# Kernel optimization log

Measured on AMD Instinct MI355X. Metric: run time of the kernel, lower is better.

The kernel has to match this reference:

```python
import jax, jax.numpy as jnp
import numpy as np

WS = 16       # window size
SHIFT = 8     # shift size
HEADS = 16
DIM = 512
HIDDEN = 2048
B, H, W = 8, 64, 64
EPS = 1e-5


def _rel_coords_table(ws):
    h = np.arange(-(ws - 1), ws, dtype=np.float32)
    t = np.stack(np.meshgrid(h, h, indexing='ij'), axis=-1)  # (2ws-1, 2ws-1, 2)
    t = t / (ws - 1) * 8.0
    t = np.sign(t) * np.log2(np.abs(t) + 1.0) / np.log2(8.0)
    return t.reshape(-1, 2)


def _rel_pos_index(ws):
    coords = np.stack(np.meshgrid(np.arange(ws), np.arange(ws), indexing='ij'))
    cf = coords.reshape(2, -1)                      # (2, N)
    rel = (cf[:, :, None] - cf[:, None, :]).transpose(1, 2, 0)  # (N, N, 2)
    rel[..., 0] += ws - 1
    rel[..., 1] += ws - 1
    rel[..., 0] *= 2 * ws - 1
    return rel.sum(-1)                              # (N, N)


def _attn_mask(h, w, ws, shift):
    img = np.zeros((h, w))
    cnt = 0
    for hs in (slice(0, -ws), slice(-ws, -shift), slice(-shift, None)):
        for wsl in (slice(0, -ws), slice(-ws, -shift), slice(-shift, None)):
            img[hs, wsl] = cnt
            cnt += 1
    mw = img.reshape(h // ws, ws, w // ws, ws).transpose(0, 2, 1, 3).reshape(-1, ws * ws)
    am = mw[:, None, :] - mw[:, :, None]            # (nW, N, N)
    return np.where(am != 0, -100.0, 0.0).astype(np.float32)


def _ln(x, g, b):
    m = x.mean(-1, keepdims=True)
    v = ((x - m) ** 2).mean(-1, keepdims=True)
    return (x - m) * jax.lax.rsqrt(v + EPS) * g + b


def setup_inputs() -> dict:
    key = jax.random.key(0)
    ks = jax.random.split(key, 16)
    s = 0.02
    return {
        'x': jax.random.normal(ks[0], (B, H, W, DIM), jnp.float32),
        'qkv_w': jax.random.normal(ks[1], (3 * DIM, DIM), jnp.float32) * s,
        'q_bias': jnp.zeros((DIM,), jnp.float32),
        'v_bias': jnp.zeros((DIM,), jnp.float32),
        'logit_scale': jnp.full((HEADS, 1, 1), np.log(10.0), jnp.float32),
        'cpb_w1': jax.random.normal(ks[2], (512, 2), jnp.float32) * s,
        'cpb_b1': jnp.zeros((512,), jnp.float32),
        'cpb_w2': jax.random.normal(ks[3], (HEADS, 512), jnp.float32) * s,
        'proj_w': jax.random.normal(ks[4], (DIM, DIM), jnp.float32) * s,
        'proj_b': jnp.zeros((DIM,), jnp.float32),
        'norm1_g': jnp.ones((DIM,), jnp.float32),
        'norm1_b': jnp.zeros((DIM,), jnp.float32),
        'norm2_g': jnp.ones((DIM,), jnp.float32),
        'norm2_b': jnp.zeros((DIM,), jnp.float32),
        'fc1_w': jax.random.normal(ks[5], (HIDDEN, DIM), jnp.float32) * s,
        'fc1_b': jnp.zeros((HIDDEN,), jnp.float32),
        'fc2_w': jax.random.normal(ks[6], (DIM, HIDDEN), jnp.float32) * s,
        'fc2_b': jnp.zeros((DIM,), jnp.float32),
    }


def reference(x, qkv_w, q_bias, v_bias, logit_scale, cpb_w1, cpb_b1, cpb_w2,
              proj_w, proj_b, norm1_g, norm1_b, norm2_g, norm2_b,
              fc1_w, fc1_b, fc2_w, fc2_b):
    b, h, w, c = x.shape
    N = WS * WS
    nW = (h // WS) * (w // WS)
    hd = c // HEADS

    # --- shifted window cosine attention ---
    shifted = jnp.roll(x, (-SHIFT, -SHIFT), axis=(1, 2))
    xw = shifted.reshape(b, h // WS, WS, w // WS, WS, c)
    xw = xw.transpose(0, 1, 3, 2, 4, 5).reshape(-1, N, c)  # (b*nW, N, C)

    bias = jnp.concatenate([q_bias, jnp.zeros_like(q_bias), v_bias])
    qkv = (xw @ qkv_w.T + bias).reshape(-1, N, 3, HEADS, hd).transpose(2, 0, 3, 1, 4)
    q, k, v = qkv[0], qkv[1], qkv[2]  # (Bn, heads, N, hd)

    qn = q / jnp.maximum(jnp.linalg.norm(q, axis=-1, keepdims=True), 1e-12)
    kn = k / jnp.maximum(jnp.linalg.norm(k, axis=-1, keepdims=True), 1e-12)
    scale = jnp.exp(jnp.minimum(logit_scale, jnp.log(jnp.float32(100.0))))  # (heads,1,1)
    attn = jnp.einsum('bhnd,bhmd->bhnm', qn, kn) * scale

    # continuous relative position bias (CPB MLP)
    table = jnp.asarray(_rel_coords_table(WS))                    # (M, 2)
    t = jax.nn.relu(table @ cpb_w1.T + cpb_b1) @ cpb_w2.T          # (M, heads)
    idx = _rel_pos_index(WS).reshape(-1)
    rpb = t[idx].reshape(N, N, HEADS).transpose(2, 0, 1)
    rpb = 16.0 * jax.nn.sigmoid(rpb)
    attn = attn + rpb[None]

    mask = jnp.asarray(_attn_mask(h, w, WS, SHIFT))                # (nW, N, N)
    attn = attn.reshape(b, nW, HEADS, N, N) + mask[None, :, None]
    attn = jax.nn.softmax(attn.reshape(-1, HEADS, N, N), axis=-1)

    out = jnp.einsum('bhnm,bhmd->bhnd', attn, v).transpose(0, 2, 1, 3).reshape(-1, N, c)
    out = out @ proj_w.T + proj_b

    out = out.reshape(b, h // WS, w // WS, WS, WS, c)
    out = out.transpose(0, 1, 3, 2, 4, 5).reshape(b, h, w, c)
    out = jnp.roll(out, (SHIFT, SHIFT), axis=(1, 2))

    # post-norm residuals (SwinV2 style)
    x = x + _ln(out, norm1_g, norm1_b)
    hmid = jax.nn.gelu(x @ fc1_w.T + fc1_b, approximate=False)
    mlp_out = hmid @ fc2_w.T + fc2_b
    x = x + _ln(mlp_out, norm2_g, norm2_b)
    return x
```

## Files before the change

### kernel.cpp

```cpp
#include <hip/hip_runtime.h>
#include <math.h>


#define HEADS 16
#define HD 32
#define NTOK 256
#define DIMC 512
#define HIDDEN 2048

typedef __attribute__((ext_vector_type(8))) short bf16x8;
typedef __attribute__((ext_vector_type(4))) float f32x4;
typedef __attribute__((ext_vector_type(8))) unsigned short ushort8;

#define MFMA16(a, b, c) __builtin_amdgcn_mfma_f32_16x16x32_bf16((a), (b), (c), 0, 0, 0)

__device__ __forceinline__ unsigned short f2bf(float f) {
  union { float f; unsigned u; } v; v.f = f;
  unsigned r = v.u + 0x7FFFu + ((v.u >> 16) & 1u);
  return (unsigned short)(r >> 16);
}
__device__ __forceinline__ float bf2f(unsigned short h) {
  union { unsigned u; float f; } v; v.u = ((unsigned)h) << 16; return v.f;
}
__device__ __forceinline__ void gload16(const void* g, void* l) {
  __builtin_amdgcn_global_load_lds(
      (const __attribute__((address_space(1))) unsigned int*)g,
      (__attribute__((address_space(3))) unsigned int*)l, 16, 0, 0);
}
__device__ __forceinline__ int band(int x) { return x < 48 ? 0 : (x < 56 ? 1 : 2); }

__device__ __forceinline__ float gelu_fast(float x) {
  float u2 = x * (1.5957691216f + 0.0713548163f * x * x);
  u2 = fminf(u2, 80.f);
  float e = __expf(u2);
  return x * (e / (e + 1.f));
}

__device__ __forceinline__ void gemm256_main(const unsigned short* Ab, const unsigned short* Bb,
                                             int K, unsigned short* aT, unsigned short* bT,
                                             f32x4 (&acc)[8][4]) {
  const int tid = threadIdx.x;
  const int w = tid >> 6, lane = tid & 63;
  const int cl = lane & 15, g = lane >> 4;
  const int wr = (w >> 2) * 128, wc = (w & 3) * 64;
  const int off0 = (2 * w) * 1024 + lane * 16;
  const int off1 = (2 * w + 1) * 1024 + lane * 16;
  const int r0 = off0 >> 6, c0 = ((off0 >> 4) & 3) ^ ((r0 >> 1) & 3);
  const int r1 = off1 >> 6, c1 = ((off1 >> 4) & 3) ^ ((r1 >> 1) & 3);
  const char* Ac = (const char*)Ab;
  const char* Bc = (const char*)Bb;
  const size_t sA0 = (size_t)r0 * (K * 2) + (size_t)c0 * 16;
  const size_t sA1 = (size_t)r1 * (K * 2) + (size_t)c1 * 16;
  const int T = K >> 5;
  gload16(Ac + sA0, (char*)aT + off0);
  gload16(Ac + sA1, (char*)aT + off1);
  gload16(Bc + sA0, (char*)bT + off0);
  gload16(Bc + sA1, (char*)bT + off1);
  __syncthreads();
  for (int t = 0; t < T; t++) {
    const int cur = (t & 1) * 8192, nxt = 8192 - cur;
    if (t + 1 < T) {
      size_t kb = (size_t)(t + 1) * 64;
      gload16(Ac + sA0 + kb, (char*)aT + nxt * 2 + off0);
      gload16(Ac + sA1 + kb, (char*)aT + nxt * 2 + off1);
      gload16(Bc + sA0 + kb, (char*)bT + nxt * 2 + off0);
      gload16(Bc + sA1 + kb, (char*)bT + nxt * 2 + off1);
    }
    bf16x8 bfv[4];
#pragma unroll
    for (int ni = 0; ni < 4; ni++) {
      int row = wc + ni * 16 + cl;
      int gs = g ^ ((row >> 1) & 3);
      bfv[ni] = *(const bf16x8*)(bT + cur + row * 32 + gs * 8);
    }
#pragma unroll
    for (int mi = 0; mi < 8; mi++) {
      int row = wr + mi * 16 + cl;
      int gs = g ^ ((row >> 1) & 3);
      bf16x8 af = *(const bf16x8*)(aT + cur + row * 32 + gs * 8);
#pragma unroll
      for (int ni = 0; ni < 4; ni++) acc[mi][ni] = MFMA16(af, bfv[ni], acc[mi][ni]);
    }
    if (t + 1 < T) __syncthreads();
  }
}

__device__ __forceinline__ void xcd_swizzle(int& bm, int& bn) {
  int gx = gridDim.x;
  int nwg = gx * gridDim.y;
  int flat = blockIdx.y * gx + blockIdx.x;
  int cpx = nwg >> 3;
  int swz = (flat & 7) * cpx + (flat >> 3);
  bm = swz % gx;
  bn = swz / gx;
}

__global__ __launch_bounds__(512, 2) void gemm_qkv(const unsigned short* A,
                                                   const unsigned short* Bw, const float* qbias,
                                                   const float* vbias, unsigned short* qo,
                                                   unsigned short* ko, unsigned short* vo) {
  __shared__ unsigned short aT[2 * 8192];
  __shared__ unsigned short bT[2 * 8192];
  int bm, bn;
  xcd_swizzle(bm, bn);
  f32x4 acc[8][4] = {};
  gemm256_main(A + (size_t)bm * 256 * DIMC, Bw + (size_t)bn * 256 * DIMC, DIMC, aT, bT, acc);
  int lane = threadIdx.x & 63, w = threadIdx.x >> 6;
  int wr = (w >> 2) * 128, wc = (w & 3) * 64, g = lane >> 4, cl = lane & 15;
  int which = bn >> 1;
  unsigned short* base = which == 0 ? qo : (which == 1 ? ko : vo);
#pragma unroll
  for (int ni = 0; ni < 4; ni++) {
    int gn = bn * 256 + wc + ni * 16 + cl;
    int wn = gn & 511, head = wn >> 5, hd = wn & 31;
    float bv = (which == 0) ? qbias[wn] : (which == 2 ? vbias[wn] : 0.f);
#pragma unroll
    for (int mi = 0; mi < 8; mi++) {
#pragma unroll
      for (int reg = 0; reg < 4; reg++) {
        int gm = bm * 256 + wr + mi * 16 + 4 * g + reg;
        int win = gm >> 8, tok = gm & 255;
        base[(((size_t)(win * HEADS + head)) * NTOK + tok) * HD + hd] =
            f2bf(acc[mi][ni][reg] + bv);
      }
    }
  }
}

template <int GELU>
__global__ __launch_bounds__(512, 2) void gemm_epi(const unsigned short* A,
                                                   const unsigned short* Bw, const float* bias,
                                                   unsigned short* out, int N, int K) {
  __shared__ unsigned short aT[2 * 8192];
  __shared__ unsigned short bT[2 * 8192];
  int bm, bn;
  xcd_swizzle(bm, bn);
  f32x4 acc[8][4] = {};
  gemm256_main(A + (size_t)bm * 256 * K, Bw + (size_t)bn * 256 * K, K, aT, bT, acc);
  int lane = threadIdx.x & 63, w = threadIdx.x >> 6;
  int wr = (w >> 2) * 128, wc = (w & 3) * 64, g = lane >> 4, cl = lane & 15;
  float bv[4];
#pragma unroll
  for (int ni = 0; ni < 4; ni++) bv[ni] = bias[bn * 256 + wc + ni * 16 + cl];
#pragma unroll
  for (int mi = 0; mi < 8; mi++) {
#pragma unroll
    for (int reg = 0; reg < 4; reg++) {
      int gm = bm * 256 + wr + mi * 16 + 4 * g + reg;
      unsigned short* rowp = out + (size_t)gm * N + bn * 256 + wc + cl;
#pragma unroll
      for (int ni = 0; ni < 4; ni++) {
        float val = acc[mi][ni][reg] + bv[ni];
        if (GELU) val = gelu_fast(val);
        rowp[ni * 16] = f2bf(val);
      }
    }
  }
}

__global__ __launch_bounds__(256) void attn_kernel(const unsigned short* qg,
                                                   const unsigned short* kg,
                                                   const unsigned short* vg, const float* rpbt,
                                                   const float* logit_scale,
                                                   unsigned short* attn_out) {
  __shared__ unsigned short kS[256 * 32];
  __shared__ unsigned short vT[32 * 256];
  __shared__ unsigned short pS[64 * 256];

  int bid = blockIdx.x;
  int qb = bid & 3, h = (bid >> 2) & 15, win = bid >> 6;
  int tid = threadIdx.x, lane = tid & 63, w = tid >> 6;
  int g = lane >> 4, cl = lane & 15;
  const size_t whbase = ((size_t)(win * HEADS + h)) * NTOK * HD;
  const unsigned short* qwin = qg + whbase + (size_t)qb * 64 * HD;
  const unsigned short* kwin = kg + whbase;
  const unsigned short* vwin = vg + whbase;

#pragma unroll
  for (int i = 0; i < 4; i++) {
    int ci = i * 256 + tid, row = ci >> 2, gc = ci & 3;
    uint4 d = *(const uint4*)(kwin + row * 32 + gc * 8);
    *(uint4*)(kS + row * 32 + ((gc ^ ((row >> 1) & 3)) * 8)) = d;
  }
  {
    int tok = tid;
    ushort8 t0 = *(const ushort8*)(vwin + tok * 32);
    ushort8 t1 = *(const ushort8*)(vwin + tok * 32 + 8);
    ushort8 t2 = *(const ushort8*)(vwin + tok * 32 + 16);
    ushort8 t3 = *(const ushort8*)(vwin + tok * 32 + 24);
    int kc = tok >> 3, ki = tok & 7;
#pragma unroll
    for (int j = 0; j < 8; j++) {
      vT[(j)*256 + ((kc ^ (j & 7)) << 3) + ki] = t0[j];
      vT[(8 + j) * 256 + ((kc ^ ((8 + j) & 7)) << 3) + ki] = t1[j];
      vT[(16 + j) * 256 + ((kc ^ ((16 + j) & 7)) << 3) + ki] = t2[j];
      vT[(24 + j) * 256 + ((kc ^ ((24 + j) & 7)) << 3) + ki] = t3[j];
    }
  }
  __syncthreads();

  float scale = __expf(fminf(logit_scale[h], 4.6051702f));

  {
    int row = tid;
    int sw = (row >> 1) & 3;
    ushort8 ch[4];
#pragma unroll
    for (int gc = 0; gc < 4; gc++) ch[gc] = *(const ushort8*)(kS + row * 32 + ((gc ^ sw) * 8));
    float ss = 0.f;
#pragma unroll
    for (int gc = 0; gc < 4; gc++)
#pragma unroll
      for (int j = 0; j < 8; j++) { float f = bf2f(ch[gc][j]); ss += f * f; }
    float rn = rsqrtf(fmaxf(ss, 1e-24f));
#pragma unroll
    for (int gc = 0; gc < 4; gc++) {
      ushort8 o;
#pragma unroll
      for (int j = 0; j < 8; j++) o[j] = f2bf(bf2f(ch[gc][j]) * rn);
      *(ushort8*)(kS + row * 32 + ((gc ^ sw) * 8)) = o;
    }
  }

  bf16x8 qf;
  {
    int qrow = 16 * w + cl;
    ushort8 qraw = *(const ushort8*)(qwin + qrow * 32 + 8 * g);
    float qe[8];
    float ss = 0.f;
#pragma unroll
    for (int j = 0; j < 8; j++) { qe[j] = bf2f(qraw[j]); ss += qe[j] * qe[j]; }
    ss += __shfl_xor(ss, 16, 64);
    ss += __shfl_xor(ss, 32, 64);
    float rn = rsqrtf(fmaxf(ss, 1e-24f)) * scale;
#pragma unroll
    for (int j = 0; j < 8; j++) qf[j] = (short)f2bf(qe[j] * rn);
  }
  __syncthreads();

  f32x4 acc[16];
#pragma unroll
  for (int ct = 0; ct < 16; ct++) {
    int kr = ct * 16 + cl;
    bf16x8 kf = *(const bf16x8*)(kS + kr * 32 + ((g ^ ((kr >> 1) & 3)) * 8));
    f32x4 z = {0.f, 0.f, 0.f, 0.f};
    acc[ct] = MFMA16(qf, kf, z);
  }

  int wh = (win >> 2) & 3, ww = win & 3;
  int bandcc = band(ww * 16 + cl);
  const float* rpbh = rpbt + h * 961;
  float m4[4];
  int baseidx[4], ridq[4];
#pragma unroll
  for (int reg = 0; reg < 4; reg++) {
    int qrow = qb * 64 + 16 * w + 4 * g + reg;
    int ri = qrow >> 4, ci = qrow & 15;
    ridq[reg] = 3 * band(wh * 16 + ri) + band(ww * 16 + ci);
    baseidx[reg] = (ri + 15) * 31 + (ci + 15 - cl);
    m4[reg] = -1e30f;
  }
#pragma unroll
  for (int ct = 0; ct < 16; ct++) {
    int brc = 3 * band(wh * 16 + ct);
#pragma unroll
    for (int reg = 0; reg < 4; reg++) {
      float v = acc[ct][reg] + rpbh[baseidx[reg] - ct * 31] +
                ((ridq[reg] != (brc + bandcc)) ? -100.f : 0.f);
      acc[ct][reg] = v;
      m4[reg] = fmaxf(m4[reg], v);
    }
  }
#pragma unroll
  for (int reg = 0; reg < 4; reg++) {
#pragma unroll
    for (int o = 1; o < 16; o <<= 1) m4[reg] = fmaxf(m4[reg], __shfl_xor(m4[reg], o, 64));
  }

  float s4[4] = {0.f, 0.f, 0.f, 0.f};
#pragma unroll
  for (int ct = 0; ct < 16; ct++) {
#pragma unroll
    for (int reg = 0; reg < 4; reg++) {
      float p = __expf(acc[ct][reg] - m4[reg]);
      s4[reg] += p;
      int row = 16 * w + 4 * g + reg;
      int c = ct * 16 + cl;
      pS[row * 256 + (((c >> 3) ^ (row & 7)) << 3) + (c & 7)] = f2bf(p);
    }
  }
#pragma unroll
  for (int reg = 0; reg < 4; reg++) {
#pragma unroll
    for (int o = 1; o < 16; o <<= 1) s4[reg] += __shfl_xor(s4[reg], o, 64);
  }

  f32x4 o0 = {0.f, 0.f, 0.f, 0.f}, o1 = {0.f, 0.f, 0.f, 0.f};
  int prow = 16 * w + cl;
#pragma unroll
  for (int ks = 0; ks < 8; ks++) {
    bf16x8 pf = *(const bf16x8*)(pS + prow * 256 + ((((ks * 4 + g)) ^ (prow & 7)) << 3));
    int kc = ks * 4 + g;
    bf16x8 vf0 = *(const bf16x8*)(vT + cl * 256 + ((kc ^ (cl & 7)) << 3));
    bf16x8 vf1 = *(const bf16x8*)(vT + (16 + cl) * 256 + ((kc ^ ((16 + cl) & 7)) << 3));
    o0 = MFMA16(pf, vf0, o0);
    o1 = MFMA16(pf, vf1, o1);
  }

#pragma unroll
  for (int reg = 0; reg < 4; reg++) {
    int row = 16 * w + 4 * g + reg;
    float linv = 1.f / s4[reg];
    size_t tokg = (size_t)win * NTOK + qb * 64 + row;
    attn_out[tokg * DIMC + h * 32 + cl] = f2bf(o0[reg] * linv);
    attn_out[tokg * DIMC + h * 32 + 16 + cl] = f2bf(o1[reg] * linv);
  }
}

__global__ __launch_bounds__(256) void cvt_bf16(const float* src, unsigned short* dst, int n8) {
  int i = blockIdx.x * 256 + threadIdx.x;
  if (i >= n8) return;
  const float* s = src + (size_t)i * 8;
  float4 a = *(const float4*)s, b = *(const float4*)(s + 4);
  ushort8 o;
  o[0] = f2bf(a.x); o[1] = f2bf(a.y); o[2] = f2bf(a.z); o[3] = f2bf(a.w);
  o[4] = f2bf(b.x); o[5] = f2bf(b.y); o[6] = f2bf(b.z); o[7] = f2bf(b.w);
  *(ushort8*)(dst + (size_t)i * 8) = o;
}

__device__ __forceinline__ float cpb_coord(int i) {
  float t = (float)(i - 15) * (8.f / 15.f);
  float s = (t > 0.f) ? 1.f : ((t < 0.f) ? -1.f : 0.f);
  return s * log2f(fabsf(t) + 1.f) * (1.f / 3.f);
}

__global__ __launch_bounds__(256) void cpb_kernel(const float* w1, const float* b1, const float* w2,
                                                  float* rpbt) {
  int i = blockIdx.x * 256 + threadIdx.x;
  if (i >= 961 * 16) return;
  int m = i >> 4, h = i & 15;
  int mi = m / 31, mj = m % 31;
  float c0 = cpb_coord(mi), c1 = cpb_coord(mj);
  float acc = 0.f;
  for (int j = 0; j < 512; j++) {
    float hv = fmaxf(w1[2 * j] * c0 + w1[2 * j + 1] * c1 + b1[j], 0.f);
    acc += hv * w2[h * 512 + j];
  }
  rpbt[h * 961 + m] = 16.f / (1.f + __expf(-acc));
}

__global__ __launch_bounds__(256) void xw_gather(const float* x, unsigned short* xw) {
  int idx = blockIdx.x * 256 + threadIdx.x;
  int m = idx >> 6, chunk = idx & 63;
  int win = m >> 8, tok = m & 255;
  int b = win >> 4, wh = (win >> 2) & 3, ww = win & 3;
  int tr = tok >> 4, tc = tok & 15;
  int sr = (wh * 16 + tr + 8) & 63, sc = (ww * 16 + tc + 8) & 63;
  const float* src = x + ((size_t)((b * 64 + sr) * 64 + sc)) * 512 + chunk * 8;
  float4 a = *(const float4*)src, bq = *(const float4*)(src + 4);
  ushort8 o;
  o[0] = f2bf(a.x); o[1] = f2bf(a.y); o[2] = f2bf(a.z); o[3] = f2bf(a.w);
  o[4] = f2bf(bq.x); o[5] = f2bf(bq.y); o[6] = f2bf(bq.z); o[7] = f2bf(bq.w);
  *(ushort8*)(xw + (size_t)m * 512 + chunk * 8) = o;
}

__global__ __launch_bounds__(256) void ln1_kernel(const unsigned short* pr, const float* x,
                                                  const float* gw, const float* bw,
                                                  unsigned short* x1b) {
  int w = threadIdx.x >> 6, lane = threadIdx.x & 63;
  size_t t = (size_t)blockIdx.x * 4 + w;
  int ti = (int)t;
  int b = ti >> 12, rc = ti & 4095, r = rc >> 6, c = rc & 63;
  int sr = (r + 56) & 63, sc = (c + 56) & 63;
  int win = b * 16 + (sr >> 4) * 4 + (sc >> 4);
  int tok = (sr & 15) * 16 + (sc & 15);
  int ch = lane * 8;
  ushort8 pv = *(const ushort8*)(pr + ((size_t)win * 256 + tok) * 512 + ch);
  float pf[8];
  float s = 0.f, s2 = 0.f;
#pragma unroll
  for (int j = 0; j < 8; j++) { pf[j] = bf2f(pv[j]); s += pf[j]; s2 += pf[j] * pf[j]; }
#pragma unroll
  for (int o = 1; o < 64; o <<= 1) { s += __shfl_xor(s, o, 64); s2 += __shfl_xor(s2, o, 64); }
  float mean = s * (1.f / 512.f);
  float rstd = rsqrtf(s2 * (1.f / 512.f) - mean * mean + 1e-5f);
  const float* xrow = x + t * 512 + ch;
  float4 xa = *(const float4*)xrow, xb = *(const float4*)(xrow + 4);
  float xs[8] = {xa.x, xa.y, xa.z, xa.w, xb.x, xb.y, xb.z, xb.w};
  ushort8 o8;
#pragma unroll
  for (int j = 0; j < 8; j++) {
    float y = (pf[j] - mean) * rstd * gw[ch + j] + bw[ch + j];
    o8[j] = f2bf(xs[j] + y);
  }
  *(ushort8*)(x1b + t * 512 + ch) = o8;
}

__global__ __launch_bounds__(256) void ln2_kernel(const unsigned short* mp,
                                                  const unsigned short* x1b, const float* gw,
                                                  const float* bw, float* out) {
  int w = threadIdx.x >> 6, lane = threadIdx.x & 63;
  size_t t = (size_t)blockIdx.x * 4 + w;
  int ch = lane * 8;
  ushort8 mv = *(const ushort8*)(mp + t * 512 + ch);
  float pf[8];
  float s = 0.f, s2 = 0.f;
#pragma unroll
  for (int j = 0; j < 8; j++) { pf[j] = bf2f(mv[j]); s += pf[j]; s2 += pf[j] * pf[j]; }
#pragma unroll
  for (int o = 1; o < 64; o <<= 1) { s += __shfl_xor(s, o, 64); s2 += __shfl_xor(s2, o, 64); }
  float mean = s * (1.f / 512.f);
  float rstd = rsqrtf(s2 * (1.f / 512.f) - mean * mean + 1e-5f);
  ushort8 xv = *(const ushort8*)(x1b + t * 512 + ch);
  float vals[8];
#pragma unroll
  for (int j = 0; j < 8; j++)
    vals[j] = bf2f(xv[j]) + (pf[j] - mean) * rstd * gw[ch + j] + bw[ch + j];
  *(float4*)(out + t * 512 + ch) = make_float4(vals[0], vals[1], vals[2], vals[3]);
  *(float4*)(out + t * 512 + ch + 4) = make_float4(vals[4], vals[5], vals[6], vals[7]);
}

extern "C" void kernel_launch(void* const* d_in, const int* in_sizes, int n_in, void* d_out,
                              int out_size, void* d_ws, size_t ws_size, hipStream_t stream) {
  (void)in_sizes; (void)n_in; (void)out_size; (void)ws_size;
  const float* x = (const float*)d_in[0];
  const float* qkv_w = (const float*)d_in[1];
  const float* q_bias = (const float*)d_in[2];
  const float* v_bias = (const float*)d_in[3];
  const float* logit_sc = (const float*)d_in[4];
  const float* cpb_w1 = (const float*)d_in[5];
  const float* cpb_b1 = (const float*)d_in[6];
  const float* cpb_w2 = (const float*)d_in[7];
  const float* proj_w = (const float*)d_in[8];
  const float* proj_b = (const float*)d_in[9];
  const float* n1g = (const float*)d_in[10];
  const float* n1b = (const float*)d_in[11];
  const float* n2g = (const float*)d_in[12];
  const float* n2b = (const float*)d_in[13];
  const float* fc1_w = (const float*)d_in[14];
  const float* fc1_b = (const float*)d_in[15];
  const float* fc2_w = (const float*)d_in[16];
  const float* fc2_b = (const float*)d_in[17];

  char* ws = (char*)d_ws;
  unsigned short* wq = (unsigned short*)(ws);
  unsigned short* wp = (unsigned short*)(ws + (2ll << 20));
  unsigned short* w1 = (unsigned short*)(ws + (4ll << 20));
  unsigned short* w2 = (unsigned short*)(ws + (8ll << 20));
  float* rpbt = (float*)(ws + (12ll << 20));
  unsigned short* xw = (unsigned short*)(ws + (16ll << 20));
  unsigned short* qbuf = (unsigned short*)(ws + (48ll << 20));
  unsigned short* kbuf = (unsigned short*)(ws + (80ll << 20));
  unsigned short* vbuf = (unsigned short*)(ws + (112ll << 20));
  unsigned short* projout = (unsigned short*)(ws + (144ll << 20));
  unsigned short* x1b = (unsigned short*)(ws + (176ll << 20));
  unsigned short* hmid = (unsigned short*)(ws + (48ll << 20));
  unsigned short* mlpout = xw;
  float* out = (float*)d_out;

  cvt_bf16<<<dim3(384), dim3(256), 0, stream>>>(qkv_w, wq, 1536 * 512 / 8);
  cvt_bf16<<<dim3(128), dim3(256), 0, stream>>>(proj_w, wp, 512 * 512 / 8);
  cvt_bf16<<<dim3(512), dim3(256), 0, stream>>>(fc1_w, w1, 2048 * 512 / 8);
  cvt_bf16<<<dim3(512), dim3(256), 0, stream>>>(fc2_w, w2, 512 * 2048 / 8);
  cpb_kernel<<<dim3(61), dim3(256), 0, stream>>>(cpb_w1, cpb_b1, cpb_w2, rpbt);
  xw_gather<<<dim3(8192), dim3(256), 0, stream>>>(x, xw);

  gemm_qkv<<<dim3(128, 6), dim3(512), 0, stream>>>(xw, wq, q_bias, v_bias, qbuf, kbuf, vbuf);
  attn_kernel<<<dim3(8192), dim3(256), 0, stream>>>(qbuf, kbuf, vbuf, rpbt, logit_sc, xw);
  gemm_epi<0><<<dim3(128, 2), dim3(512), 0, stream>>>(xw, wp, proj_b, projout, 512, 512);
  ln1_kernel<<<dim3(8192), dim3(256), 0, stream>>>(projout, x, n1g, n1b, x1b);

  gemm_epi<1><<<dim3(128, 8), dim3(512), 0, stream>>>(x1b, w1, fc1_b, hmid, 2048, 512);
  gemm_epi<0><<<dim3(128, 2), dim3(512), 0, stream>>>(hmid, w2, fc2_b, mlpout, 512, 2048);
  ln2_kernel<<<dim3(8192), dim3(256), 0, stream>>>(mlpout, x1b, n2g, n2b, out);
}
```

Baseline: 560.8 us.

## Deepen GEMM LDS pipeline to four stages with vmcnt waits; reorder XCD swizzle

Replaces the double-buffered GEMM main loop with a four-slot ring that keeps three tile loads in flight. Explicit s_waitcnt vmcnt counts and a single barrier per iteration replace the two __syncthreads calls, so global-to-LDS latency is hidden behind more MFMA work. The XCD swizzle now maps consecutive indices along the N dimension, which changes which tiles share L2 per chiplet. Static LDS use rises to 128KB per block for the QKV and epilogue GEMMs, which may reduce the two-blocks-per-CU occupancy requested by the launch bounds.

```diff
diff --git a/kernel.cpp b/kernel.cpp
--- a/kernel.cpp
+++ b/kernel.cpp
@@ -13,6 +13,7 @@
 typedef __attribute__((ext_vector_type(8))) unsigned short ushort8;
 
 #define MFMA16(a, b, c) __builtin_amdgcn_mfma_f32_16x16x32_bf16((a), (b), (c), 0, 0, 0)
+#define WAIT_VM(N) asm volatile("s_waitcnt vmcnt(" #N ")" ::: "memory")
 
 __device__ __forceinline__ unsigned short f2bf(float f) {
   union { float f; unsigned u; } v; v.f = f;
@@ -52,20 +53,30 @@
   const size_t sA0 = (size_t)r0 * (K * 2) + (size_t)c0 * 16;
   const size_t sA1 = (size_t)r1 * (K * 2) + (size_t)c1 * 16;
   const int T = K >> 5;
-  gload16(Ac + sA0, (char*)aT + off0);
-  gload16(Ac + sA1, (char*)aT + off1);
-  gload16(Bc + sA0, (char*)bT + off0);
-  gload16(Bc + sA1, (char*)bT + off1);
-  __syncthreads();
+#pragma unroll
+  for (int p = 0; p < 3; p++) {
+    size_t kb = (size_t)p * 64;
+    int bo = p * 16384;
+    gload16(Ac + sA0 + kb, (char*)aT + bo + off0);
+    gload16(Ac + sA1 + kb, (char*)aT + bo + off1);
+    gload16(Bc + sA0 + kb, (char*)bT + bo + off0);
+    gload16(Bc + sA1 + kb, (char*)bT + bo + off1);
+  }
   for (int t = 0; t < T; t++) {
-    const int cur = (t & 1) * 8192, nxt = 8192 - cur;
-    if (t + 1 < T) {
-      size_t kb = (size_t)(t + 1) * 64;
-      gload16(Ac + sA0 + kb, (char*)aT + nxt * 2 + off0);
-      gload16(Ac + sA1 + kb, (char*)aT + nxt * 2 + off1);
-      gload16(Bc + sA0 + kb, (char*)bT + nxt * 2 + off0);
-      gload16(Bc + sA1 + kb, (char*)bT + nxt * 2 + off1);
-    }
+    if (t + 3 <= T) WAIT_VM(8);
+    else if (t + 2 == T) WAIT_VM(4);
+    else WAIT_VM(0);
+    __builtin_amdgcn_s_barrier();
+    asm volatile("" ::: "memory");
+    if (t + 3 < T) {
+      size_t kb = (size_t)(t + 3) * 64;
+      int bo = ((t + 3) & 3) * 16384;
+      gload16(Ac + sA0 + kb, (char*)aT + bo + off0);
+      gload16(Ac + sA1 + kb, (char*)aT + bo + off1);
+      gload16(Bc + sA0 + kb, (char*)bT + bo + off0);
+      gload16(Bc + sA1 + kb, (char*)bT + bo + off1);
+    }
+    const int cur = (t & 3) * 8192;
     bf16x8 bfv[4];
 #pragma unroll
     for (int ni = 0; ni < 4; ni++) {
@@ -81,26 +92,25 @@
 #pragma unroll
       for (int ni = 0; ni < 4; ni++) acc[mi][ni] = MFMA16(af, bfv[ni], acc[mi][ni]);
     }
-    if (t + 1 < T) __syncthreads();
   }
 }
 
 __device__ __forceinline__ void xcd_swizzle(int& bm, int& bn) {
-  int gx = gridDim.x;
-  int nwg = gx * gridDim.y;
-  int flat = blockIdx.y * gx + blockIdx.x;
+  int gy = gridDim.y;
+  int nwg = gridDim.x * gy;
+  int flat = blockIdx.y * gridDim.x + blockIdx.x;
   int cpx = nwg >> 3;
   int swz = (flat & 7) * cpx + (flat >> 3);
-  bm = swz % gx;
-  bn = swz / gx;
+  bm = swz / gy;
+  bn = swz % gy;
 }
 
 __global__ __launch_bounds__(512, 2) void gemm_qkv(const unsigned short* A,
                                                    const unsigned short* Bw, const float* qbias,
                                                    const float* vbias, unsigned short* qo,
                                                    unsigned short* ko, unsigned short* vo) {
-  __shared__ unsigned short aT[2 * 8192];
-  __shared__ unsigned short bT[2 * 8192];
+  __shared__ unsigned short aT[4 * 8192];
+  __shared__ unsigned short bT[4 * 8192];
   int bm, bn;
   xcd_swizzle(bm, bn);
   f32x4 acc[8][4] = {};
@@ -131,8 +141,8 @@
 __global__ __launch_bounds__(512, 2) void gemm_epi(const unsigned short* A,
                                                    const unsigned short* Bw, const float* bias,
                                                    unsigned short* out, int N, int K) {
-  __shared__ unsigned short aT[2 * 8192];
-  __shared__ unsigned short bT[2 * 8192];
+  __shared__ unsigned short aT[4 * 8192];
+  __shared__ unsigned short bT[4 * 8192];
   int bm, bn;
   xcd_swizzle(bm, bn);
   f32x4 acc[8][4] = {};
```

After: 549.8 us. About the same (-2.0%).
